# Kernel tuning notes

Hardware: AMD Instinct MI355X
Metric: run time of the kernel (lower is better)

## Reference

```python
import jax, jax.numpy as jnp
import numpy as np
from jax import lax

D_MODEL = 384; EXPAND = 2; D_INNER = EXPAND * D_MODEL; D_STATE = 14; D_CONV = 4
DT_RANK = (D_MODEL + 15) // 16  # 24
DEPTH = 4; NUM_CLASSES = 3
BS = 2; T = 16; IMG = 224; PATCH = 16; PH = IMG // PATCH; NPATCH = PH * PH  # 196


def setup_inputs() -> dict:
    key = jax.random.key(0)
    ks = jax.random.split(key, 16)
    def rn(k, shape, sc=0.02):
        return jax.random.normal(k, shape, jnp.float32) * sc
    inp = {}
    inp['x'] = jax.random.normal(ks[0], (BS, T, 3, IMG, IMG), jnp.float32)
    inp['patch_w'] = rn(ks[1], (D_MODEL, 3, PATCH, PATCH))
    inp['patch_b'] = jnp.zeros((D_MODEL,), jnp.float32)
    inp['ln1_g'] = jnp.ones((DEPTH, D_MODEL), jnp.float32)
    inp['ln1_b'] = jnp.zeros((DEPTH, D_MODEL), jnp.float32)
    inp['in_w'] = rn(ks[2], (DEPTH, 2 * D_INNER, D_MODEL))
    inp['conv_w'] = rn(ks[3], (DEPTH, D_INNER, D_CONV), 0.1)
    inp['conv_b'] = jnp.zeros((DEPTH, D_INNER), jnp.float32)
    inp['xproj_w'] = rn(ks[4], (DEPTH, DT_RANK + 2 * D_STATE, D_INNER))
    inp['dt_w'] = rn(ks[5], (DEPTH, D_INNER, DT_RANK), 0.1)
    inp['dt_b'] = jnp.full((DEPTH, D_INNER), -4.6, jnp.float32)  # softplus(-4.6) ~ 0.01
    # S4D-real init: A = [1..d_state] per channel
    inp['A_log'] = jnp.log(jnp.tile(jnp.arange(1, D_STATE + 1, dtype=jnp.float32), (DEPTH, D_INNER, 1)))
    inp['Dparam'] = jnp.ones((DEPTH, D_INNER), jnp.float32)
    inp['out_w'] = rn(ks[6], (DEPTH, D_MODEL, D_INNER))
    inp['ln2_g'] = jnp.ones((DEPTH, D_MODEL), jnp.float32)
    inp['ln2_b'] = jnp.zeros((DEPTH, D_MODEL), jnp.float32)
    inp['fc1_w'] = rn(ks[7], (DEPTH, 4 * D_MODEL, D_MODEL))
    inp['fc1_b'] = jnp.zeros((DEPTH, 4 * D_MODEL), jnp.float32)
    inp['fc2_w'] = rn(ks[8], (DEPTH, D_MODEL, 4 * D_MODEL))
    inp['fc2_b'] = jnp.zeros((DEPTH, D_MODEL), jnp.float32)
    inp['head_w'] = rn(ks[9], (NUM_CLASSES, D_MODEL))
    inp['head_b'] = jnp.zeros((NUM_CLASSES,), jnp.float32)
    return inp


def _layernorm(x, g, b):
    mu = jnp.mean(x, -1, keepdims=True)
    v = jnp.mean((x - mu) ** 2, -1, keepdims=True)
    return (x - mu) * lax.rsqrt(v + 1e-5) * g + b


def _silu(x):
    return x * jax.nn.sigmoid(x)


def _mamba(u, in_w, conv_w, conv_b, xproj_w, dt_w, dt_b, A_log, Dp, out_w):
    b, L, _ = u.shape
    xz = jnp.einsum('bld,ed->ble', u, in_w)            # (b, L, 2*d_inner)
    xi, z = jnp.split(xz, 2, axis=-1)
    # causal depthwise conv1d along L
    xpad = jnp.pad(xi, ((0, 0), (D_CONV - 1, 0), (0, 0)))
    xc = conv_b + sum(conv_w[:, k] * xpad[:, k:k + L, :] for k in range(D_CONV))
    xc = _silu(xc)                                      # (b, L, d_inner)
    dbl = jnp.einsum('ble,re->blr', xc, xproj_w)
    dt = jax.nn.softplus(jnp.einsum('blr,dr->bld', dbl[..., :DT_RANK], dt_w) + dt_b)
    Bm = dbl[..., DT_RANK:DT_RANK + D_STATE]            # (b, L, n)
    Cm = dbl[..., DT_RANK + D_STATE:]                   # (b, L, n)
    A = -jnp.exp(A_log)                                 # (d_inner, n)

    def step(h, inps):
        dt_t, B_t, C_t, x_t = inps                      # (b,d),(b,n),(b,n),(b,d)
        h = jnp.exp(dt_t[..., None] * A) * h + (dt_t * x_t)[..., None] * B_t[:, None, :]
        return h, jnp.einsum('bdn,bn->bd', h, C_t)

    h0 = jnp.zeros((b, D_INNER, D_STATE), u.dtype)
    _, ys = lax.scan(step, h0, (jnp.swapaxes(dt, 0, 1), jnp.swapaxes(Bm, 0, 1),
                                jnp.swapaxes(Cm, 0, 1), jnp.swapaxes(xc, 0, 1)))
    y = jnp.swapaxes(ys, 0, 1) + Dp * xc
    y = y * _silu(z)
    return jnp.einsum('ble,de->bld', y, out_w)


def reference(x, patch_w, patch_b, ln1_g, ln1_b, in_w, conv_w, conv_b, xproj_w, dt_w,
              dt_b, A_log, Dparam, out_w, ln2_g, ln2_b, fc1_w, fc1_b, fc2_w, fc2_b,
              head_w, head_b):
    bs, t = x.shape[:2]
    N = bs * t
    # patch embed: stride==kernel conv -> unfold + matmul
    xf = x.reshape(N, 3, PH, PATCH, PH, PATCH).transpose(0, 2, 4, 1, 3, 5).reshape(N, NPATCH, 3 * PATCH * PATCH)
    emb = xf @ patch_w.reshape(D_MODEL, -1).T + patch_b  # (N, 196, d_model)
    h = emb.reshape(bs, t * NPATCH, D_MODEL)
    for i in range(DEPTH):
        h = h + _mamba(_layernorm(h, ln1_g[i], ln1_b[i]), in_w[i], conv_w[i], conv_b[i],
                       xproj_w[i], dt_w[i], dt_b[i], A_log[i], Dparam[i], out_w[i])
        m = _layernorm(h, ln2_g[i], ln2_b[i])
        m = jax.nn.gelu(m @ fc1_w[i].T + fc1_b[i], approximate=True) @ fc2_w[i].T + fc2_b[i]
        h = h + m
    h = h.reshape(bs, t, NPATCH, D_MODEL)
    pooled = h.max(axis=2)                               # pool='max' over patch dim
    return pooled @ head_w.T + head_b                    # (bs, t, num_classes)
```

## Files before the change

kernel.cpp:

```cpp
#include <hip/hip_runtime.h>
#include <hip/hip_bf16.h>
#include <math.h>

#define D_MODEL 384
#define D_INNER 768
#define D_STATE 14
#define D_CONV 4
#define DT_RANK 24
#define DEPTH 4
#define BS 2
#define LSEQ 3136
#define NROWS 6272
#define NFRAMES 32
#define NPATCH 196
#define NC 224
#define LC 14
#define GSCAN (BS*NC*D_INNER)
#define XPJ_KS 4
#define DBL_STRIDE 802816

enum { ACT_NONE = 0, ACT_GELU = 1, ACT_SOFTPLUS = 2 };
enum { OM_F32 = 0, OM_ATOMIC = 1, OM_BF16 = 2, OM_SPLITB = 3, OM_XPROJ = 4 };

typedef unsigned short u16;
typedef __attribute__((ext_vector_type(8))) short bf16x8;
typedef __attribute__((ext_vector_type(4))) float f32x4;

__device__ __forceinline__ void cp16(const void* g, void* l) {
    __builtin_amdgcn_global_load_lds((const __attribute__((address_space(1))) char*)g,
                                     (__attribute__((address_space(3))) char*)l, 16, 0, 0);
}
__device__ __forceinline__ float bf2f(__hip_bfloat16 v) { return __bfloat162float(v); }
__device__ __forceinline__ float us2f(unsigned short u) {
    unsigned int w = ((unsigned int)u) << 16;
    return __uint_as_float(w);
}

__device__ __forceinline__ void pow_tree(float e1, float* pw) {
    float e2 = e1 * e1, e4 = e2 * e2, e8 = e4 * e4;
    pw[0] = e1;       pw[1] = e2;       pw[2] = e2 * e1;  pw[3] = e4;
    pw[4] = e4 * e1;  pw[5] = e4 * e2;  pw[6] = e4 * pw[2]; pw[7] = e8;
    pw[8] = e8 * e1;  pw[9] = e8 * e2;  pw[10] = e8 * pw[2]; pw[11] = e8 * e4;
    pw[12] = e8 * pw[4]; pw[13] = e8 * pw[5];
}

#define CVT_N0 294912
#define CVT_N1 2359296
#define CVT_N2 1179648
#define CVT_N3 2359296
#define CVT_N4 2359296
#define CVT_TOT (CVT_N0+CVT_N1+CVT_N2+CVT_N3+CVT_N4)
#define XPJ_TOT (DEPTH*128*768)
__global__ __launch_bounds__(256) void cvt_all_k(const float* __restrict__ s0,
                                                 const float* __restrict__ s1,
                                                 const float* __restrict__ s2,
                                                 const float* __restrict__ s3,
                                                 const float* __restrict__ s4,
                                                 const float* __restrict__ xproj_w,
                                                 __hip_bfloat16* __restrict__ d,
                                                 __hip_bfloat16* __restrict__ xpj_pad) {
    int t = blockIdx.x * 256 + threadIdx.x;
    int i = t * 4;
    if (i < CVT_TOT) {
        const float* s;
        int off;
        if (i < CVT_N0) { s = s0; off = i; }
        else if (i < CVT_N0 + CVT_N1) { s = s1; off = i - CVT_N0; }
        else if (i < CVT_N0 + CVT_N1 + CVT_N2) { s = s2; off = i - CVT_N0 - CVT_N1; }
        else if (i < CVT_N0 + CVT_N1 + CVT_N2 + CVT_N3) { s = s3; off = i - CVT_N0 - CVT_N1 - CVT_N2; }
        else { s = s4; off = i - CVT_N0 - CVT_N1 - CVT_N2 - CVT_N3; }
        float4 v = *(const float4*)(s + off);
        d[i + 0] = __float2bfloat16(v.x);
        d[i + 1] = __float2bfloat16(v.y);
        d[i + 2] = __float2bfloat16(v.z);
        d[i + 3] = __float2bfloat16(v.w);
    }
    if (t < XPJ_TOT) {
        int l = t / (128 * 768), rem = t % (128 * 768);
        int n = rem / 768, k = rem % 768;
        float v = (n < 52) ? xproj_w[(size_t)l * 52 * 768 + n * 768 + k] : 0.f;
        xpj_pad[t] = __float2bfloat16(v);
    }
}

__global__ __launch_bounds__(256) void pack_patches(const float* __restrict__ x,
                                                    __hip_bfloat16* __restrict__ xf) {
    int idx4 = blockIdx.x * 256 + threadIdx.x;
    int k = (idx4 % 192) * 4;
    int row = idx4 / 192;
    int p = row % NPATCH;
    int f = row / NPATCH;
    int c = k >> 8, i = (k >> 4) & 15, j = k & 15;
    int ph = p / 14, pw = p % 14;
    float4 v = *(const float4*)(x + ((size_t)(f * 3 + c) * 224 + ph * 16 + i) * 224 + pw * 16 + j);
    __hip_bfloat16* o = xf + (size_t)row * 768 + k;
    o[0] = __float2bfloat16(v.x);
    o[1] = __float2bfloat16(v.y);
    o[2] = __float2bfloat16(v.z);
    o[3] = __float2bfloat16(v.w);
}

template <int ACT, int OM, int NX, int NY, int KSPLIT, int BK>
__global__ __launch_bounds__(256) void gemm_mfma(const u16* __restrict__ A, int lda,
                                                 const u16* __restrict__ B, int ldb,
                                                 const float* __restrict__ bias,
                                                 void* __restrict__ Cp, void* __restrict__ Cp2,
                                                 int ldc, int K) {
    constexpr int NXK = NX * KSPLIT;
    constexpr int NSUB = BK / 32;
    const int e = blockIdx.x & 7;
    const int sblk = blockIdx.x >> 3;
    const int y0 = (e * NY) >> 3;
    const int y1 = ((e + 1) * NY) >> 3;
    if (sblk >= (y1 - y0) * NXK) return;
    const int m0 = (y0 + sblk / NXK) * 128;
    const int xe = sblk % NXK;
    const int n0 = (xe % NX) * 128;
    const int kh = xe / NX;
    const int Keff = K / KSPLIT;

    __shared__ u16 As[NSUB * 4096];
    __shared__ u16 Bs[NSUB * 4096];
    const int tid = threadIdx.x;
    const int wave = tid >> 6;
    const int lane = tid & 63;
    const int quad = lane >> 4;
    const int l16 = lane & 15;
    const int wr = (wave >> 1) * 64;
    const int wc = (wave & 1) * 64;

    const int u0 = wave * 128 + lane;
    const int u1 = u0 + 64;
    const int r0 = u0 >> 2, c0 = (u0 & 3) * 8;
    const int r1 = u1 >> 2, c1 = (u1 & 3) * 8;
    const u16* ga0 = A + (size_t)(m0 + r0) * lda + kh * Keff + c0;
    const u16* ga1 = A + (size_t)(m0 + r1) * lda + kh * Keff + c1;
    const u16* gb0 = B + (size_t)(n0 + r0) * ldb + kh * Keff + c0;
    const u16* gb1 = B + (size_t)(n0 + r1) * ldb + kh * Keff + c1;
    u16* As0 = As + wave * 1024;
    u16* As1 = As0 + 512;
    u16* Bs0 = Bs + wave * 1024;
    u16* Bs1 = Bs0 + 512;

    f32x4 acc[4][4];
#pragma unroll
    for (int i = 0; i < 4; ++i)
#pragma unroll
        for (int j = 0; j < 4; ++j) acc[i][j] = (f32x4){0.f, 0.f, 0.f, 0.f};

    for (int kt = 0; kt < Keff; kt += BK) {
#pragma unroll
        for (int ss = 0; ss < NSUB; ++ss) {
            cp16(ga0 + kt + ss * 32, As0 + ss * 4096);
            cp16(ga1 + kt + ss * 32, As1 + ss * 4096);
            cp16(gb0 + kt + ss * 32, Bs0 + ss * 4096);
            cp16(gb1 + kt + ss * 32, Bs1 + ss * 4096);
        }
        __syncthreads();
#pragma unroll
        for (int ss = 0; ss < NSUB; ++ss) {
            bf16x8 af[4], bfr[4];
#pragma unroll
            for (int i = 0; i < 4; ++i)
                af[i] = *(const bf16x8*)&As[ss * 4096 + (wr + i * 16 + l16) * 32 + quad * 8];
#pragma unroll
            for (int j = 0; j < 4; ++j)
                bfr[j] = *(const bf16x8*)&Bs[ss * 4096 + (wc + j * 16 + l16) * 32 + quad * 8];
#pragma unroll
            for (int i = 0; i < 4; ++i)
#pragma unroll
                for (int j = 0; j < 4; ++j)
                    acc[i][j] = __builtin_amdgcn_mfma_f32_16x16x32_bf16(af[i], bfr[j], acc[i][j], 0, 0, 0);
        }
        __syncthreads();
    }

    float* Cf = (float*)Cp;
    __hip_bfloat16* Cb = (__hip_bfloat16*)Cp;
    __hip_bfloat16* Cb2 = (__hip_bfloat16*)Cp2;
#pragma unroll
    for (int j = 0; j < 4; ++j) {
        const int gn = n0 + wc + j * 16 + l16;
        const float bsv = (bias && kh == 0) ? bias[gn] : 0.f;
#pragma unroll
        for (int i = 0; i < 4; ++i) {
            const int gm = m0 + wr + i * 16 + quad * 4;
#pragma unroll
            for (int r = 0; r < 4; ++r) {
                float v = acc[i][j][r] + bsv;
                if (ACT == ACT_GELU) {
                    float t2 = 1.5957691216057308f * (v + 0.044715f * v * v * v);
                    v = v / (1.f + __expf(-t2));
                } else if (ACT == ACT_SOFTPLUS) {
                    v = (v > 20.f) ? v : log1pf(__expf(v));
                }
                const int gr = gm + r;
                if (OM == OM_SPLITB) {
                    if (gn < D_INNER) Cb[(size_t)gr * D_INNER + gn] = __float2bfloat16(v);
                    else Cb2[(size_t)gr * D_INNER + gn - D_INNER] = __float2bfloat16(v);
                } else if (OM == OM_XPROJ) {
                    Cf[(size_t)kh * DBL_STRIDE + (size_t)gr * 128 + gn] = v;
                } else if (OM == OM_ATOMIC) {
                    atomicAdd(&Cf[(size_t)gr * ldc + gn], v);
                } else {
                    size_t o = (size_t)gr * ldc + gn;
                    if (OM == OM_BF16) Cb[o] = __float2bfloat16(v);
                    else Cf[o] = v;
                }
            }
        }
    }
}

__global__ __launch_bounds__(256) void layernorm_k(const float* __restrict__ x,
                                                   const float* __restrict__ g,
                                                   const float* __restrict__ b,
                                                   __hip_bfloat16* __restrict__ o) {
    int wid = blockIdx.x * 4 + (threadIdx.x >> 6);
    int lane = threadIdx.x & 63;
    const float* xr = x + (size_t)wid * D_MODEL;
    float v[6];
    float s = 0.f;
#pragma unroll
    for (int i = 0; i < 6; ++i) { v[i] = xr[lane + i * 64]; s += v[i]; }
#pragma unroll
    for (int off = 1; off < 64; off <<= 1) s += __shfl_xor(s, off, 64);
    float mean = s * (1.f / 384.f);
    float q = 0.f;
#pragma unroll
    for (int i = 0; i < 6; ++i) { float t = v[i] - mean; q += t * t; }
#pragma unroll
    for (int off = 1; off < 64; off <<= 1) q += __shfl_xor(q, off, 64);
    float rs = rsqrtf(q * (1.f / 384.f) + 1e-5f);
    __hip_bfloat16* orow = o + (size_t)wid * D_MODEL;
#pragma unroll
    for (int i = 0; i < 6; ++i) {
        int d = lane + i * 64;
        orow[d] = __float2bfloat16((v[i] - mean) * rs * g[d] + b[d]);
    }
}

__global__ __launch_bounds__(256) void conv_silu_k(const __hip_bfloat16* __restrict__ xxb,
                                                   const float* __restrict__ w,
                                                   const float* __restrict__ bias,
                                                   __hip_bfloat16* __restrict__ xcb) {
    int idx4 = blockIdx.x * 256 + threadIdx.x;
    int e = (idx4 % 192) * 4;
    int row = idx4 / 192;
    int l = row % LSEQ;
    float4 bv = *(const float4*)(bias + e);
    float acc[4] = {bv.x, bv.y, bv.z, bv.w};
    float4 w0 = *(const float4*)(w + (e + 0) * 4);
    float4 w1 = *(const float4*)(w + (e + 1) * 4);
    float4 w2 = *(const float4*)(w + (e + 2) * 4);
    float4 w3 = *(const float4*)(w + (e + 3) * 4);
    const float wv[4][4] = {{w0.x, w0.y, w0.z, w0.w}, {w1.x, w1.y, w1.z, w1.w},
                            {w2.x, w2.y, w2.z, w2.w}, {w3.x, w3.y, w3.z, w3.w}};
#pragma unroll
    for (int k = 0; k < 4; ++k) {
        if (l - 3 + k >= 0) {
            ushort4 xv = *(const ushort4*)(xxb + (size_t)(row + k - 3) * D_INNER + e);
            acc[0] += wv[0][k] * us2f(xv.x);
            acc[1] += wv[1][k] * us2f(xv.y);
            acc[2] += wv[2][k] * us2f(xv.z);
            acc[3] += wv[3][k] * us2f(xv.w);
        }
    }
    ushort4 ov;
    {
        float sg0 = 1.f / (1.f + __expf(-acc[0]));
        float sg1 = 1.f / (1.f + __expf(-acc[1]));
        float sg2 = 1.f / (1.f + __expf(-acc[2]));
        float sg3 = 1.f / (1.f + __expf(-acc[3]));
        __hip_bfloat16 b0 = __float2bfloat16(acc[0] * sg0);
        __hip_bfloat16 b1 = __float2bfloat16(acc[1] * sg1);
        __hip_bfloat16 b2 = __float2bfloat16(acc[2] * sg2);
        __hip_bfloat16 b3 = __float2bfloat16(acc[3] * sg3);
        ov.x = *(unsigned short*)&b0; ov.y = *(unsigned short*)&b1;
        ov.z = *(unsigned short*)&b2; ov.w = *(unsigned short*)&b3;
    }
    *(ushort4*)(xcb + (size_t)row * D_INNER + e) = ov;
}

__global__ __launch_bounds__(256) void scan_stage1(const __hip_bfloat16* __restrict__ xcb,
                                                   const float* __restrict__ dbl,
                                                   const float* __restrict__ dtw,
                                                   const float* __restrict__ dtb,
                                                   float* __restrict__ E1V,
                                                   float* __restrict__ UV,
                                                   float* __restrict__ P,
                                                   float* __restrict__ S) {
    __shared__ float sX[LC][40];
    int g = blockIdx.x * 256 + threadIdx.x;
    int d = g % D_INNER;
    int bc = g / D_INNER;
    int c = bc % NC, b = bc / NC;
    long rowbase = (long)b * LSEQ + c * LC;
    for (int t = threadIdx.x; t < LC * 40; t += 256) {
        int lr = t / 40, col = t % 40;
        size_t o = (size_t)(rowbase + lr) * 128 + col;
        float v = 0.f;
#pragma unroll
        for (int q = 0; q < XPJ_KS; ++q) v += dbl[(size_t)q * DBL_STRIDE + o];
        sX[lr][col] = v;
    }
    float wt[DT_RANK];
#pragma unroll
    for (int r = 0; r < DT_RANK; ++r) wt[r] = dtw[(size_t)d * DT_RANK + r];
    const float dbias = dtb[d];
    __syncthreads();
    float h[D_STATE], p[D_STATE];
#pragma unroll
    for (int n = 0; n < D_STATE; ++n) { h[n] = 0.f; p[n] = 1.f; }
#pragma unroll 2
    for (int lr = 0; lr < LC; ++lr) {
        long row = rowbase + lr;
        float raw = dbias;
#pragma unroll
        for (int q = 0; q < 6; ++q) {
            f32x4 xv4 = *(const f32x4*)&sX[lr][4 * q];
            raw += xv4[0] * wt[4 * q] + xv4[1] * wt[4 * q + 1]
                 + xv4[2] * wt[4 * q + 2] + xv4[3] * wt[4 * q + 3];
        }
        float er = __expf(raw);
        float dtv = (raw > 20.f) ? raw : __logf(1.f + er);
        float xv = bf2f(xcb[row * D_INNER + d]);
        float u = dtv * xv;
        float e1 = __expf(-dtv);
        E1V[row * D_INNER + d] = e1;
        UV[row * D_INNER + d] = u;
        float Bv[16];
        *(f32x4*)(Bv + 0)  = *(const f32x4*)&sX[lr][24];
        *(f32x4*)(Bv + 4)  = *(const f32x4*)&sX[lr][28];
        *(f32x4*)(Bv + 8)  = *(const f32x4*)&sX[lr][32];
        *(f32x4*)(Bv + 12) = *(const f32x4*)&sX[lr][36];
        float pw[D_STATE];
        pow_tree(e1, pw);
#pragma unroll
        for (int n = 0; n < D_STATE; ++n) {
            p[n] *= pw[n];
            h[n] = pw[n] * h[n] + u * Bv[n];
        }
    }
#pragma unroll
    for (int n = 0; n < D_STATE; ++n) { P[n * GSCAN + g] = p[n]; S[n * GSCAN + g] = h[n]; }
}

__global__ __launch_bounds__(256) void scan_stage2(const float* __restrict__ P,
                                                   float* __restrict__ S) {
    int g = blockIdx.x * 256 + threadIdx.x;
    int n = g / (BS * D_INNER);
    int rem = g % (BS * D_INNER);
    int b = rem / D_INNER, d = rem % D_INNER;
    const float* Pn = P + (size_t)n * GSCAN;
    float* Sn = S + (size_t)n * GSCAN;
    float h = 0.f;
    int idx = b * NC * D_INNER + d;
#pragma unroll 8
    for (int c = 0; c < NC; ++c, idx += D_INNER) {
        float pv = Pn[idx];
        float sv = Sn[idx];
        Sn[idx] = h;
        h = pv * h + sv;
    }
}

__global__ __launch_bounds__(256) void scan_stage3(const __hip_bfloat16* __restrict__ xcb,
                                                   const __hip_bfloat16* __restrict__ zb,
                                                   const float* __restrict__ dbl,
                                                   const float* __restrict__ E1V,
                                                   const float* __restrict__ UV,
                                                   const float* __restrict__ Dp,
                                                   const float* __restrict__ HI,
                                                   __hip_bfloat16* __restrict__ yb) {
    __shared__ float sBC[LC][28];
    int g = blockIdx.x * 256 + threadIdx.x;
    int d = g % D_INNER;
    int bc = g / D_INNER;
    int c = bc % NC, b = bc / NC;
    long rowbase = (long)b * LSEQ + c * LC;
    for (int t = threadIdx.x; t < LC * 28; t += 256) {
        int lr = t / 28, col = t % 28;
        size_t o = (size_t)(rowbase + lr) * 128 + 24 + col;
        float v = 0.f;
#pragma unroll
        for (int q = 0; q < XPJ_KS; ++q) v += dbl[(size_t)q * DBL_STRIDE + o];
        sBC[lr][col] = v;
    }
    __syncthreads();
    float h[D_STATE];
#pragma unroll
    for (int n = 0; n < D_STATE; ++n) h[n] = HI[n * GSCAN + g];
    float Dd = Dp[d];
#pragma unroll 2
    for (int lr = 0; lr < LC; ++lr) {
        long row = rowbase + lr;
        float e1 = E1V[row * D_INNER + d];
        float u  = UV[row * D_INNER + d];
        float xv = bf2f(xcb[row * D_INNER + d]);
        float zv = bf2f(zb[row * D_INNER + d]);
        float BC[28];
#pragma unroll
        for (int q = 0; q < 7; ++q)
            *(f32x4*)(BC + q * 4) = *(const f32x4*)&sBC[lr][q * 4];
        float pw[D_STATE];
        pow_tree(e1, pw);
        float acc = 0.f;
#pragma unroll
        for (int n = 0; n < D_STATE; ++n) {
            h[n] = pw[n] * h[n] + u * BC[n];
            acc += h[n] * BC[14 + n];
        }
        float yv = acc + Dd * xv;
        float sg = 1.f / (1.f + __expf(-zv));
        yb[row * D_INNER + d] = __float2bfloat16(yv * (zv * sg));
    }
}

__global__ __launch_bounds__(256) void pool_part_k(const float* __restrict__ h,
                                                   float* __restrict__ ppart) {
    int idx = blockIdx.x * 256 + threadIdx.x;
    int cch = idx / (NFRAMES * D_MODEL);
    int rem = idx % (NFRAMES * D_MODEL);
    int f = rem / D_MODEL, d = rem % D_MODEL;
    int p0 = cch * 49;
    const float* hp = h + ((size_t)f * NPATCH + p0) * D_MODEL + d;
    float m = -1e30f;
#pragma unroll 7
    for (int p = 0; p < 49; ++p) m = fmaxf(m, hp[(size_t)p * D_MODEL]);
    ppart[idx] = m;
}

__global__ __launch_bounds__(64) void head_k(const float* __restrict__ ppart,
                                             const float* __restrict__ hw,
                                             const float* __restrict__ hb,
                                             float* __restrict__ out) {
    int o = blockIdx.x;
    int f = o / 3, cls = o % 3;
    int lane = threadIdx.x;
    const int FD = NFRAMES * D_MODEL;
    float s = 0.f;
    for (int d = lane; d < D_MODEL; d += 64) {
        int base = f * D_MODEL + d;
        float m = fmaxf(fmaxf(ppart[base], ppart[FD + base]),
                        fmaxf(ppart[2 * FD + base], ppart[3 * FD + base]));
        s += m * hw[cls * D_MODEL + d];
    }
#pragma unroll
    for (int off = 1; off < 64; off <<= 1) s += __shfl_xor(s, off, 64);
    if (lane == 0) out[o] = s + hb[cls];
}

extern "C" void kernel_launch(void* const* d_in, const int* in_sizes, int n_in,
                              void* d_out, int out_size, void* d_ws, size_t ws_size,
                              hipStream_t stream) {
    const float* x       = (const float*)d_in[0];
    const float* patch_w = (const float*)d_in[1];
    const float* patch_b = (const float*)d_in[2];
    const float* ln1_g   = (const float*)d_in[3];
    const float* ln1_b   = (const float*)d_in[4];
    const float* in_w    = (const float*)d_in[5];
    const float* conv_w  = (const float*)d_in[6];
    const float* conv_b  = (const float*)d_in[7];
    const float* xproj_w = (const float*)d_in[8];
    const float* dt_w    = (const float*)d_in[9];
    const float* dt_b    = (const float*)d_in[10];
    const float* Dparam  = (const float*)d_in[12];
    const float* out_w   = (const float*)d_in[13];
    const float* ln2_g   = (const float*)d_in[14];
    const float* ln2_b   = (const float*)d_in[15];
    const float* fc1_w   = (const float*)d_in[16];
    const float* fc1_b   = (const float*)d_in[17];
    const float* fc2_w   = (const float*)d_in[18];
    const float* fc2_b   = (const float*)d_in[19];
    const float* head_w  = (const float*)d_in[20];
    const float* head_b  = (const float*)d_in[21];

    float* ws = (float*)d_ws;
    float* H     = ws;
    __hip_bfloat16* XZxb = (__hip_bfloat16*)(H + 2408448);
    __hip_bfloat16* XZzb = XZxb + 4816896;
    __hip_bfloat16* XCb  = XZzb + 4816896;
    float* DBL   = (float*)(XCb + 4816896);
    __hip_bfloat16* MIDb = (__hip_bfloat16*)(DBL + (size_t)XPJ_KS * DBL_STRIDE);
    __hip_bfloat16* Ub   = MIDb + 9633792;
    __hip_bfloat16* Yb   = Ub + 2408448;
    float* P     = (float*)(Yb + 4816896);
    float* S     = P + (size_t)D_STATE * GSCAN;
    float* E1V   = S + (size_t)D_STATE * GSCAN;
    float* UV    = E1V + 4816896;
    float* PPART = UV + 4816896;
    __hip_bfloat16* Wb = (__hip_bfloat16*)(PPART + 49152);
    __hip_bfloat16* Wb_patch = Wb;
    __hip_bfloat16* Wb_in    = Wb_patch + 294912;
    __hip_bfloat16* Wb_out   = Wb_in + 2359296;
    __hip_bfloat16* Wb_fc1   = Wb_out + 1179648;
    __hip_bfloat16* Wb_fc2   = Wb_fc1 + 2359296;
    __hip_bfloat16* Wb_xpj   = Wb_fc2 + 2359296;
    __hip_bfloat16* XFb  = XZxb;

    dim3 blk(256);
    const int G12  = 8 * 7 * 12;
    const int G3   = 8 * 7 * 3;
    const int G3K2 = 8 * 7 * 3 * 2;
    const int G1K4 = 8 * 7 * 1 * XPJ_KS;

    cvt_all_k<<<(CVT_TOT / 4 + 255) / 256, blk, 0, stream>>>(
        patch_w, in_w, out_w, fc1_w, fc2_w, xproj_w, Wb_patch, Wb_xpj);

    pack_patches<<<4704, blk, 0, stream>>>(x, XFb);
    gemm_mfma<ACT_NONE, OM_F32, 3, 49, 1, 64><<<G3, blk, 0, stream>>>(
        (const u16*)XFb, 768, (const u16*)Wb_patch, 768, patch_b, H, nullptr, D_MODEL, 768);

    for (int i = 0; i < DEPTH; ++i) {
        const float* cw   = conv_w + (size_t)i * D_INNER * D_CONV;
        const float* cb   = conv_b + (size_t)i * D_INNER;
        const float* dtw  = dt_w + (size_t)i * D_INNER * DT_RANK;
        const float* dtb  = dt_b + (size_t)i * D_INNER;
        const float* Dpar = Dparam + (size_t)i * D_INNER;

        layernorm_k<<<NROWS / 4, blk, 0, stream>>>(H, ln1_g + i * D_MODEL, ln1_b + i * D_MODEL, Ub);
        gemm_mfma<ACT_NONE, OM_SPLITB, 12, 49, 1, 64><<<G12, blk, 0, stream>>>(
            (const u16*)Ub, 384, (const u16*)(Wb_in + (size_t)i * 1536 * 384), 384,
            nullptr, XZxb, XZzb, D_INNER, 384);
        conv_silu_k<<<4704, blk, 0, stream>>>(XZxb, cw, cb, XCb);
        gemm_mfma<ACT_NONE, OM_XPROJ, 1, 49, XPJ_KS, 64><<<G1K4, blk, 0, stream>>>(
            (const u16*)XCb, 768, (const u16*)(Wb_xpj + (size_t)i * 128 * 768), 768,
            nullptr, DBL, nullptr, 128, 768);
        scan_stage1<<<GSCAN / 256, blk, 0, stream>>>(XCb, DBL, dtw, dtb, E1V, UV, P, S);
        scan_stage2<<<(D_STATE * BS * D_INNER) / 256, blk, 0, stream>>>(P, S);
        scan_stage3<<<GSCAN / 256, blk, 0, stream>>>(XCb, XZzb, DBL, E1V, UV, Dpar, S, Yb);
        gemm_mfma<ACT_NONE, OM_ATOMIC, 3, 49, 2, 64><<<G3K2, blk, 0, stream>>>(
            (const u16*)Yb, 768, (const u16*)(Wb_out + (size_t)i * 384 * 768), 768,
            nullptr, H, nullptr, D_MODEL, 768);

        layernorm_k<<<NROWS / 4, blk, 0, stream>>>(H, ln2_g + i * D_MODEL, ln2_b + i * D_MODEL, Ub);
        gemm_mfma<ACT_GELU, OM_BF16, 12, 49, 1, 64><<<G12, blk, 0, stream>>>(
            (const u16*)Ub, 384, (const u16*)(Wb_fc1 + (size_t)i * 1536 * 384), 384,
            fc1_b + (size_t)i * 4 * D_MODEL, MIDb, nullptr, 4 * D_MODEL, 384);
        gemm_mfma<ACT_NONE, OM_ATOMIC, 3, 49, 2, 64><<<G3K2, blk, 0, stream>>>(
            (const u16*)MIDb, 1536, (const u16*)(Wb_fc2 + (size_t)i * 384 * 1536), 1536,
            fc2_b + (size_t)i * D_MODEL, H, nullptr, D_MODEL, 1536);
    }

    pool_part_k<<<192, blk, 0, stream>>>(H, PPART);
    head_k<<<NFRAMES * 3, dim3(64), 0, stream>>>(PPART, head_w, head_b, (float*)d_out);
}
```

Before: 943.6 us.

## Double-buffer GEMM K loop and replace atomic split-K with partial buffers

The GEMM main loop now uses two 32-wide LDS stages with manual waitcnt and barrier placement, so the next sub-tile's global-to-LDS loads overlap the MFMA work on the current one. The out-proj and fc2 GEMMs switch from atomicAdd split-K (2 ways) to 4-way split-K that writes plain partial sums into separate buffers. Those partials are summed into the residual stream inside the next layernorm kernel, and in the final pooling kernel. This removes atomic contention and adds parallelism, at the cost of extra partial-buffer memory traffic and hand-written synchronisation that is easy to get wrong.

New measurement: 994.7 us. 1.05x slower.

```diff
diff --git a/kernel.cpp b/kernel.cpp
--- a/kernel.cpp
+++ b/kernel.cpp
@@ -18,9 +18,10 @@
 #define GSCAN (BS*NC*D_INNER)
 #define XPJ_KS 4
 #define DBL_STRIDE 802816
+#define PART_STRIDE 2408448
 
 enum { ACT_NONE = 0, ACT_GELU = 1, ACT_SOFTPLUS = 2 };
-enum { OM_F32 = 0, OM_ATOMIC = 1, OM_BF16 = 2, OM_SPLITB = 3, OM_XPROJ = 4 };
+enum { OM_F32 = 0, OM_PARTK = 1, OM_BF16 = 2, OM_SPLITB = 3, OM_XPROJ = 4 };
 
 typedef unsigned short u16;
 typedef __attribute__((ext_vector_type(8))) short bf16x8;
@@ -100,14 +101,13 @@
     o[3] = __float2bfloat16(v.w);
 }
 
-template <int ACT, int OM, int NX, int NY, int KSPLIT, int BK>
+template <int ACT, int OM, int NX, int NY, int KSPLIT>
 __global__ __launch_bounds__(256) void gemm_mfma(const u16* __restrict__ A, int lda,
                                                  const u16* __restrict__ B, int ldb,
                                                  const float* __restrict__ bias,
                                                  void* __restrict__ Cp, void* __restrict__ Cp2,
                                                  int ldc, int K) {
     constexpr int NXK = NX * KSPLIT;
-    constexpr int NSUB = BK / 32;
     const int e = blockIdx.x & 7;
     const int sblk = blockIdx.x >> 3;
     const int y0 = (e * NY) >> 3;
@@ -119,8 +119,8 @@
     const int kh = xe / NX;
     const int Keff = K / KSPLIT;
 
-    __shared__ u16 As[NSUB * 4096];
-    __shared__ u16 Bs[NSUB * 4096];
+    __shared__ u16 As[2 * 4096];
+    __shared__ u16 Bs[2 * 4096];
     const int tid = threadIdx.x;
     const int wave = tid >> 6;
     const int lane = tid & 63;
@@ -148,31 +148,49 @@
 #pragma unroll
         for (int j = 0; j < 4; ++j) acc[i][j] = (f32x4){0.f, 0.f, 0.f, 0.f};
 
-    for (int kt = 0; kt < Keff; kt += BK) {
-#pragma unroll
-        for (int ss = 0; ss < NSUB; ++ss) {
-            cp16(ga0 + kt + ss * 32, As0 + ss * 4096);
-            cp16(ga1 + kt + ss * 32, As1 + ss * 4096);
-            cp16(gb0 + kt + ss * 32, Bs0 + ss * 4096);
-            cp16(gb1 + kt + ss * 32, Bs1 + ss * 4096);
-        }
-        __syncthreads();
-#pragma unroll
-        for (int ss = 0; ss < NSUB; ++ss) {
-            bf16x8 af[4], bfr[4];
-#pragma unroll
-            for (int i = 0; i < 4; ++i)
-                af[i] = *(const bf16x8*)&As[ss * 4096 + (wr + i * 16 + l16) * 32 + quad * 8];
+    auto stage = [&](int ss, int kt) {
+        cp16(ga0 + kt + ss * 32, As0 + ss * 4096);
+        cp16(ga1 + kt + ss * 32, As1 + ss * 4096);
+        cp16(gb0 + kt + ss * 32, Bs0 + ss * 4096);
+        cp16(gb1 + kt + ss * 32, Bs1 + ss * 4096);
+    };
+    auto compute = [&](int ss) {
+        bf16x8 af[4], bfr[4];
+#pragma unroll
+        for (int i = 0; i < 4; ++i)
+            af[i] = *(const bf16x8*)&As[ss * 4096 + (wr + i * 16 + l16) * 32 + quad * 8];
+#pragma unroll
+        for (int j = 0; j < 4; ++j)
+            bfr[j] = *(const bf16x8*)&Bs[ss * 4096 + (wc + j * 16 + l16) * 32 + quad * 8];
+#pragma unroll
+        for (int i = 0; i < 4; ++i)
 #pragma unroll
             for (int j = 0; j < 4; ++j)
-                bfr[j] = *(const bf16x8*)&Bs[ss * 4096 + (wc + j * 16 + l16) * 32 + quad * 8];
-#pragma unroll
-            for (int i = 0; i < 4; ++i)
-#pragma unroll
-                for (int j = 0; j < 4; ++j)
-                    acc[i][j] = __builtin_amdgcn_mfma_f32_16x16x32_bf16(af[i], bfr[j], acc[i][j], 0, 0, 0);
-        }
-        __syncthreads();
+                acc[i][j] = __builtin_amdgcn_mfma_f32_16x16x32_bf16(af[i], bfr[j], acc[i][j], 0, 0, 0);
+    };
+
+    stage(0, 0);
+    stage(1, 0);
+    for (int kt = 0; kt < Keff; kt += 64) {
+        const bool last = (kt + 64 >= Keff);
+        asm volatile("s_waitcnt vmcnt(4)" ::: "memory");
+        asm volatile("s_barrier" ::: "memory");
+        compute(0);
+        asm volatile("s_waitcnt lgkmcnt(0)" ::: "memory");
+        asm volatile("s_barrier" ::: "memory");
+        if (!last) {
+            stage(0, kt + 64);
+            asm volatile("s_waitcnt vmcnt(4)" ::: "memory");
+        } else {
+            asm volatile("s_waitcnt vmcnt(0)" ::: "memory");
+        }
+        asm volatile("s_barrier" ::: "memory");
+        compute(1);
+        if (!last) {
+            asm volatile("s_waitcnt lgkmcnt(0)" ::: "memory");
+            asm volatile("s_barrier" ::: "memory");
+            stage(1, kt + 64);
+        }
     }
 
     float* Cf = (float*)Cp;
@@ -200,8 +218,8 @@
                     else Cb2[(size_t)gr * D_INNER + gn - D_INNER] = __float2bfloat16(v);
                 } else if (OM == OM_XPROJ) {
                     Cf[(size_t)kh * DBL_STRIDE + (size_t)gr * 128 + gn] = v;
-                } else if (OM == OM_ATOMIC) {
-                    atomicAdd(&Cf[(size_t)gr * ldc + gn], v);
+                } else if (OM == OM_PARTK) {
+                    Cf[(size_t)kh * PART_STRIDE + (size_t)gr * ldc + gn] = v;
                 } else {
                     size_t o = (size_t)gr * ldc + gn;
                     if (OM == OM_BF16) Cb[o] = __float2bfloat16(v);
@@ -212,17 +230,31 @@
     }
 }
 
+template <int NPART>
 __global__ __launch_bounds__(256) void layernorm_k(const float* __restrict__ x,
+                                                   const float* __restrict__ part,
                                                    const float* __restrict__ g,
                                                    const float* __restrict__ b,
+                                                   float* __restrict__ xout,
                                                    __hip_bfloat16* __restrict__ o) {
     int wid = blockIdx.x * 4 + (threadIdx.x >> 6);
     int lane = threadIdx.x & 63;
-    const float* xr = x + (size_t)wid * D_MODEL;
+    const size_t base = (size_t)wid * D_MODEL;
     float v[6];
     float s = 0.f;
 #pragma unroll
-    for (int i = 0; i < 6; ++i) { v[i] = xr[lane + i * 64]; s += v[i]; }
+    for (int i = 0; i < 6; ++i) {
+        size_t idx = base + lane + i * 64;
+        float t = x[idx];
+#pragma unroll
+        for (int q = 0; q < NPART; ++q) t += part[(size_t)q * PART_STRIDE + idx];
+        v[i] = t;
+        s += t;
+    }
+    if (NPART > 0) {
+#pragma unroll
+        for (int i = 0; i < 6; ++i) xout[base + lane + i * 64] = v[i];
+    }
 #pragma unroll
     for (int off = 1; off < 64; off <<= 1) s += __shfl_xor(s, off, 64);
     float mean = s * (1.f / 384.f);
@@ -232,7 +264,7 @@
 #pragma unroll
     for (int off = 1; off < 64; off <<= 1) q += __shfl_xor(q, off, 64);
     float rs = rsqrtf(q * (1.f / 384.f) + 1e-5f);
-    __hip_bfloat16* orow = o + (size_t)wid * D_MODEL;
+    __hip_bfloat16* orow = o + base;
 #pragma unroll
     for (int i = 0; i < 6; ++i) {
         int d = lane + i * 64;
@@ -418,16 +450,22 @@
 }
 
 __global__ __launch_bounds__(256) void pool_part_k(const float* __restrict__ h,
+                                                   const float* __restrict__ part,
                                                    float* __restrict__ ppart) {
     int idx = blockIdx.x * 256 + threadIdx.x;
     int cch = idx / (NFRAMES * D_MODEL);
     int rem = idx % (NFRAMES * D_MODEL);
     int f = rem / D_MODEL, d = rem % D_MODEL;
     int p0 = cch * 49;
-    const float* hp = h + ((size_t)f * NPATCH + p0) * D_MODEL + d;
+    size_t base = ((size_t)f * NPATCH + p0) * D_MODEL + d;
     float m = -1e30f;
 #pragma unroll 7
-    for (int p = 0; p < 49; ++p) m = fmaxf(m, hp[(size_t)p * D_MODEL]);
+    for (int p = 0; p < 49; ++p) {
+        size_t idx2 = base + (size_t)p * D_MODEL;
+        float s = h[idx2] + part[idx2] + part[PART_STRIDE + idx2]
+                + part[2 * (size_t)PART_STRIDE + idx2] + part[3 * (size_t)PART_STRIDE + idx2];
+        m = fmaxf(m, s);
+    }
     ppart[idx] = m;
 }
 
@@ -489,7 +527,8 @@
     float* S     = P + (size_t)D_STATE * GSCAN;
     float* E1V   = S + (size_t)D_STATE * GSCAN;
     float* UV    = E1V + 4816896;
-    float* PPART = UV + 4816896;
+    float* PK    = UV + 4816896;
+    float* PPART = PK + 4 * (size_t)PART_STRIDE;
     __hip_bfloat16* Wb = (__hip_bfloat16*)(PPART + 49152);
     __hip_bfloat16* Wb_patch = Wb;
     __hip_bfloat16* Wb_in    = Wb_patch + 294912;
@@ -502,14 +541,14 @@
     dim3 blk(256);
     const int G12  = 8 * 7 * 12;
     const int G3   = 8 * 7 * 3;
-    const int G3K2 = 8 * 7 * 3 * 2;
+    const int G3K4 = 8 * 7 * 3 * 4;
     const int G1K4 = 8 * 7 * 1 * XPJ_KS;
 
     cvt_all_k<<<(CVT_TOT / 4 + 255) / 256, blk, 0, stream>>>(
         patch_w, in_w, out_w, fc1_w, fc2_w, xproj_w, Wb_patch, Wb_xpj);
 
     pack_patches<<<4704, blk, 0, stream>>>(x, XFb);
-    gemm_mfma<ACT_NONE, OM_F32, 3, 49, 1, 64><<<G3, blk, 0, stream>>>(
+    gemm_mfma<ACT_NONE, OM_F32, 3, 49, 1><<<G3, blk, 0, stream>>>(
         (const u16*)XFb, 768, (const u16*)Wb_patch, 768, patch_b, H, nullptr, D_MODEL, 768);
 
     for (int i = 0; i < DEPTH; ++i) {
@@ -519,30 +558,36 @@
         const float* dtb  = dt_b + (size_t)i * D_INNER;
         const float* Dpar = Dparam + (size_t)i * D_INNER;
 
-        layernorm_k<<<NROWS / 4, blk, 0, stream>>>(H, ln1_g + i * D_MODEL, ln1_b + i * D_MODEL, Ub);
-        gemm_mfma<ACT_NONE, OM_SPLITB, 12, 49, 1, 64><<<G12, blk, 0, stream>>>(
+        if (i == 0)
+            layernorm_k<0><<<NROWS / 4, blk, 0, stream>>>(H, nullptr,
+                ln1_g + i * D_MODEL, ln1_b + i * D_MODEL, nullptr, Ub);
+        else
+            layernorm_k<4><<<NROWS / 4, blk, 0, stream>>>(H, PK,
+                ln1_g + i * D_MODEL, ln1_b + i * D_MODEL, H, Ub);
+        gemm_mfma<ACT_NONE, OM_SPLITB, 12, 49, 1><<<G12, blk, 0, stream>>>(
             (const u16*)Ub, 384, (const u16*)(Wb_in + (size_t)i * 1536 * 384), 384,
             nullptr, XZxb, XZzb, D_INNER, 384);
         conv_silu_k<<<4704, blk, 0, stream>>>(XZxb, cw, cb, XCb);
-        gemm_mfma<ACT_NONE, OM_XPROJ, 1, 49, XPJ_KS, 64><<<G1K4, blk, 0, stream>>>(
+        gemm_mfma<ACT_NONE, OM_XPROJ, 1, 49, XPJ_KS><<<G1K4, blk, 0, stream>>>(
             (const u16*)XCb, 768, (const u16*)(Wb_xpj + (size_t)i * 128 * 768), 768,
             nullptr, DBL, nullptr, 128, 768);
         scan_stage1<<<GSCAN / 256, blk, 0, stream>>>(XCb, DBL, dtw, dtb, E1V, UV, P, S);
         scan_stage2<<<(D_STATE * BS * D_INNER) / 256, blk, 0, stream>>>(P, S);
         scan_stage3<<<GSCAN / 256, blk, 0, stream>>>(XCb, XZzb, DBL, E1V, UV, Dpar, S, Yb);
-        gemm_mfma<ACT_NONE, OM_ATOMIC, 3, 49, 2, 64><<<G3K2, blk, 0, stream>>>(
+        gemm_mfma<ACT_NONE, OM_PARTK, 3, 49, 4><<<G3K4, blk, 0, stream>>>(
             (const u16*)Yb, 768, (const u16*)(Wb_out + (size_t)i * 384 * 768), 768,
-            nullptr, H, nullptr, D_MODEL, 768);
-
-        layernorm_k<<<NROWS / 4, blk, 0, stream>>>(H, ln2_g + i * D_MODEL, ln2_b + i * D_MODEL, Ub);
-        gemm_mfma<ACT_GELU, OM_BF16, 12, 49, 1, 64><<<G12, blk, 0, stream>>>(
+            nullptr, PK, nullptr, D_MODEL, 768);
+
+        layernorm_k<4><<<NROWS / 4, blk, 0, stream>>>(H, PK,
+            ln2_g + i * D_MODEL, ln2_b + i * D_MODEL, H, Ub);
+        gemm_mfma<ACT_GELU, OM_BF16, 12, 49, 1><<<G12, blk, 0, stream>>>(
             (const u16*)Ub, 384, (const u16*)(Wb_fc1 + (size_t)i * 1536 * 384), 384,
             fc1_b + (size_t)i * 4 * D_MODEL, MIDb, nullptr, 4 * D_MODEL, 384);
-        gemm_mfma<ACT_NONE, OM_ATOMIC, 3, 49, 2, 64><<<G3K2, blk, 0, stream>>>(
+        gemm_mfma<ACT_NONE, OM_PARTK, 3, 49, 4><<<G3K4, blk, 0, stream>>>(
             (const u16*)MIDb, 1536, (const u16*)(Wb_fc2 + (size_t)i * 384 * 1536), 1536,
-            fc2_b + (size_t)i * D_MODEL, H, nullptr, D_MODEL, 1536);
-    }
-
-    pool_part_k<<<192, blk, 0, stream>>>(H, PPART);
+            fc2_b + (size_t)i * D_MODEL, PK, nullptr, D_MODEL, 1536);
+    }
+
+    pool_part_k<<<192, blk, 0, stream>>>(H, PK, PPART);
     head_k<<<NFRAMES * 3, dim3(64), 0, stream>>>(PPART, head_w, head_b, (float*)d_out);
 }
```
